# Kernel optimization log

Hardware: AMD Instinct MI355X
Metric: run time of the kernel (lower is better)

The kernel has to match this reference:

```python
import jax, jax.numpy as jnp
import numpy as np

B, S, P, E, H, NCTX = 4, 1024, 1024, 1024, 16, 2048
D = E // H


def setup_inputs() -> dict:
    key = jax.random.key(0)
    k0, k1, k2, k3 = jax.random.split(key, 4)
    x = jax.random.normal(k0, (B, S, E), jnp.float32)
    layer_past = jax.random.normal(k1, (2, B, H, P, D), jnp.float32)
    w_attn = jax.random.normal(k2, (E, 3 * E), jnp.float32) * 0.02
    b_attn = jnp.zeros((3 * E,), jnp.float32)
    w_proj = jax.random.normal(k3, (E, E), jnp.float32) * 0.02
    b_proj = jnp.zeros((E,), jnp.float32)
    return {"x": x, "layer_past": layer_past, "w_attn": w_attn,
            "b_attn": b_attn, "w_proj": w_proj, "b_proj": b_proj}


def reference(x, layer_past, w_attn, b_attn, w_proj, b_proj):
    # c_attn: Conv1D == linear with weight [nx, nf]
    qkv = x @ w_attn + b_attn                       # [B,S,3E]
    q, k, v = jnp.split(qkv, 3, axis=-1)

    def heads(t):                                   # [B,S,E] -> [B,H,S,D]
        return t.reshape(B, -1, H, D).transpose(0, 2, 1, 3)

    q, k, v = heads(q), heads(k), heads(v)
    # KV-cache concat: layer_past[0] is [B,H,P,D] (module transposes to
    # [B,H,D,P] then concats on last dim; equivalent to concat on seq dim).
    k = jnp.concatenate([layer_past[0], k], axis=2)  # [B,H,ns,D]
    v = jnp.concatenate([layer_past[1], v], axis=2)  # [B,H,ns,D]
    present = jnp.stack([k, v])                      # [2,B,H,ns,D]

    nd, ns = q.shape[2], k.shape[2]
    w = jnp.einsum('bhqd,bhkd->bhqk', q, k) / jnp.sqrt(jnp.float32(D))
    mask = jnp.tril(jnp.ones((NCTX, NCTX), jnp.float32))[ns - nd:ns, :ns]
    w = w * mask - 10000.0 * (1.0 - mask)
    a = jnp.einsum('bhqk,bhkd->bhqd', jax.nn.softmax(w, axis=-1), v)
    a = a.transpose(0, 2, 1, 3).reshape(B, -1, E)    # merge heads
    out = a @ w_proj + b_proj
    return out, present
```

## Files before the change

### kernel.cpp

```cpp
#include <hip/hip_runtime.h>
#include <hip/hip_bf16.h>

#define BB 4
#define SS 1024
#define PP 1024
#define EE 1024
#define HH 16
#define DD 64
#define NS 2048
#define E3 3072
#define VOFF 8388608
#define VPAST 4194304

typedef __attribute__((ext_vector_type(8))) short short8;
typedef __attribute__((ext_vector_type(4))) float floatx4;
typedef __attribute__((ext_vector_type(16))) float floatx16;
typedef __attribute__((ext_vector_type(4))) unsigned uintx4;

__device__ __forceinline__ short f2bf(float f) {
    return (short)(__bfloat16_as_ushort(__float2bfloat16(f)));
}

__device__ __forceinline__ unsigned cvtpk(float lo, float hi) {
    unsigned r;
    asm("v_cvt_pk_bf16_f32 %0, %1, %2" : "=v"(r) : "v"(lo), "v"(hi));
    return r;
}

__device__ __forceinline__ void plswap(unsigned &a, unsigned &b) {
    asm("v_permlane32_swap_b32 %0, %1" : "+v"(a), "+v"(b));
}

__device__ __forceinline__ void gload16(const void* g, void* l) {
    __builtin_amdgcn_global_load_lds(
        (const __attribute__((address_space(1))) void*)g,
        (__attribute__((address_space(3))) void*)l, 16, 0, 0);
}

__global__ __launch_bounds__(256) void cvt_copy_k(
    const float* __restrict__ x, const float* __restrict__ past,
    short* __restrict__ xb, short* __restrict__ kbp, short* __restrict__ vbp,
    float* __restrict__ present)
{
    size_t e0 = ((size_t)blockIdx.x * 256 + threadIdx.x) * 8;
    if (e0 < 4194304) {
        float4 a0 = *(const float4*)(x + e0);
        float4 a1 = *(const float4*)(x + e0 + 4);
        short8 s;
        s[0] = f2bf(a0.x); s[1] = f2bf(a0.y); s[2] = f2bf(a0.z); s[3] = f2bf(a0.w);
        s[4] = f2bf(a1.x); s[5] = f2bf(a1.y); s[6] = f2bf(a1.z); s[7] = f2bf(a1.w);
        *(short8*)(xb + e0) = s;
    } else {
        size_t r = e0 - 4194304;
        int sec = (r >= 4194304);
        if (sec) r -= 4194304;
        const float* src = past + (sec ? VPAST : 0) + r;
        int row = (int)(r >> 6);
        int bh = row >> 10, t = row & 1023, d = (int)(r & 63);
        size_t off = ((size_t)bh * NS + t) * DD + d;
        float4 a0 = *(const float4*)src;
        float4 a1 = *(const float4*)(src + 4);
        short8 s;
        s[0] = f2bf(a0.x); s[1] = f2bf(a0.y); s[2] = f2bf(a0.z); s[3] = f2bf(a0.w);
        s[4] = f2bf(a1.x); s[5] = f2bf(a1.y); s[6] = f2bf(a1.z); s[7] = f2bf(a1.w);
        *(short8*)((sec ? vbp : kbp) + off) = s;
        float* pd = present + (sec ? VOFF : 0) + off;
        *(float4*)(pd)     = a0;
        *(float4*)(pd + 4) = a1;
    }
}

__global__ __launch_bounds__(256) void wtrans_k(
    const float* __restrict__ wa, const float* __restrict__ wp,
    short* __restrict__ wab, short* __restrict__ wpb)
{
    __shared__ short Ts[64][72];
    int bid = blockIdx.x;
    const float* src; short* dst; int n0, k0, Nsrc;
    if (bid < 768) { k0 = (bid & 15) * 64; n0 = (bid >> 4) * 64; src = wa; dst = wab; Nsrc = E3; }
    else { bid -= 768; k0 = (bid & 15) * 64; n0 = (bid >> 4) * 64; src = wp; dst = wpb; Nsrc = EE; }
    int tid = threadIdx.x;
    int r = tid >> 2, c = (tid & 3) * 16;
    const float* s = src + (size_t)(k0 + r) * Nsrc + n0 + c;
    float4 a0 = *(const float4*)(s);
    float4 a1 = *(const float4*)(s + 4);
    float4 a2 = *(const float4*)(s + 8);
    float4 a3 = *(const float4*)(s + 12);
    Ts[c +  0][r] = f2bf(a0.x); Ts[c +  1][r] = f2bf(a0.y);
    Ts[c +  2][r] = f2bf(a0.z); Ts[c +  3][r] = f2bf(a0.w);
    Ts[c +  4][r] = f2bf(a1.x); Ts[c +  5][r] = f2bf(a1.y);
    Ts[c +  6][r] = f2bf(a1.z); Ts[c +  7][r] = f2bf(a1.w);
    Ts[c +  8][r] = f2bf(a2.x); Ts[c +  9][r] = f2bf(a2.y);
    Ts[c + 10][r] = f2bf(a2.z); Ts[c + 11][r] = f2bf(a2.w);
    Ts[c + 12][r] = f2bf(a3.x); Ts[c + 13][r] = f2bf(a3.y);
    Ts[c + 14][r] = f2bf(a3.z); Ts[c + 15][r] = f2bf(a3.w);
    __syncthreads();
    int n = tid >> 2, kc = (tid & 3) * 16;
    short8 v0 = *(const short8*)&Ts[n][kc];
    short8 v1 = *(const short8*)&Ts[n][kc + 8];
    short* d = dst + (size_t)(n0 + n) * EE + k0 + kc;
    *(short8*)d = v0;
    *(short8*)(d + 8) = v1;
}

template<int MODE>
__global__ __launch_bounds__(256) void gemm_bt_k(
    const short* __restrict__ A,
    const short* __restrict__ Bt,
    const float* __restrict__ bias,
    float* __restrict__ outf,
    short* __restrict__ qb, short* __restrict__ kbp, short* __restrict__ vbp,
    float* __restrict__ present,
    int N)
{
    __shared__ __align__(16) short As[128 * 32];
    __shared__ __align__(16) short Bs[128 * 32];
    int tid = threadIdx.x;
    int wave = tid >> 6, lane = tid & 63;
    int fr = lane & 15, quad = lane >> 4;
    int wm = wave >> 1, wn = wave & 1;
    int hw = blockIdx.y * gridDim.x + blockIdx.x;
    int nwg = gridDim.x * gridDim.y;
    int work = (hw & 7) * (nwg >> 3) + (hw >> 3);
    int bx = work / gridDim.y, by = work - bx * gridDim.y;
    int m0 = bx * 128, n0 = by * 128;

    floatx4 acc[4][4];
#pragma unroll
    for (int m = 0; m < 4; ++m)
#pragma unroll
        for (int n = 0; n < 4; ++n) acc[m][n] = (floatx4){0.f, 0.f, 0.f, 0.f};

    for (int k0 = 0; k0 < 1024; k0 += 32) {
        __syncthreads();
#pragma unroll
        for (int p = 0; p < 2; ++p) {
            int idx = p * 256 + tid;
            int row = idx >> 2, ch = idx & 3;
            gload16(A + (size_t)(m0 + row) * 1024 + k0 + ch * 8,
                    As + (p * 256 + wave * 64) * 8);
            gload16(Bt + (size_t)(n0 + row) * 1024 + k0 + ch * 8,
                    Bs + (p * 256 + wave * 64) * 8);
        }
        __syncthreads();
        short8 af[4], bf[4];
#pragma unroll
        for (int m = 0; m < 4; ++m)
            af[m] = *(const short8*)(As + (wm * 64 + m * 16 + fr) * 32 + quad * 8);
#pragma unroll
        for (int n = 0; n < 4; ++n)
            bf[n] = *(const short8*)(Bs + (wn * 64 + n * 16 + fr) * 32 + quad * 8);
#pragma unroll
        for (int m = 0; m < 4; ++m)
#pragma unroll
            for (int n = 0; n < 4; ++n)
                acc[m][n] = __builtin_amdgcn_mfma_f32_16x16x32_bf16(af[m], bf[n], acc[m][n], 0, 0, 0);
    }
#pragma unroll
    for (int n = 0; n < 4; ++n) {
        int gc = n0 + wn * 64 + n * 16 + fr;
        float bv = bias[gc];
#pragma unroll
        for (int m = 0; m < 4; ++m) {
#pragma unroll
            for (int r = 0; r < 4; ++r) {
                int gr = m0 + wm * 64 + m * 16 + quad * 4 + r;
                float val = acc[m][n][r] + bv;
                if (MODE == 1) {
                    outf[(size_t)gr * N + gc] = val;
                } else {
                    int sec = gc >> 10, h = (gc >> 6) & 15, d = gc & 63;
                    int b = gr >> 10, sq = gr & 1023;
                    size_t bh = (size_t)(b * HH + h);
                    if (sec == 0) {
                        qb[(bh * SS + sq) * DD + d] = f2bf(val * 0.125f);
                    } else {
                        size_t off = (bh * NS + PP + sq) * DD + d;
                        if (sec == 1) { present[off] = val;        kbp[off] = f2bf(val); }
                        else          { present[VOFF + off] = val; vbp[off] = f2bf(val); }
                    }
                }
            }
        }
    }
}

__global__ __launch_bounds__(256) void flash_attn_k(
    const short* __restrict__ qb, const short* __restrict__ kbp,
    const short* __restrict__ vbp, short* __restrict__ ab)
{
    __shared__ __align__(16) short smem[9216];
    short* Ks = smem;
    short* Vs = smem + 4096;

    int tid = threadIdx.x;
    int wave = tid >> 6, lane = tid & 63;
    int qcol = lane & 31, hi = lane >> 5;

    int bid = blockIdx.x;
    int work = (bid & 7) * 64 + (bid >> 3);
    int bh = work >> 3;
    int q0 = (work & 7) * 128;

    const short* qrow = qb + ((size_t)bh * SS + q0 + wave * 32 + qcol) * DD + hi * 8;
    short8 qf[4];
#pragma unroll
    for (int i = 0; i < 4; ++i) qf[i] = *(const short8*)(qrow + i * 16);

    const short* kbase = kbp + (size_t)bh * NS * DD;
    const short* vbase = vbp + (size_t)bh * NS * DD;

    float m_r = -1e30f, l_r = 0.f;
    floatx16 Oa[2];
#pragma unroll
    for (int dt = 0; dt < 2; ++dt)
#pragma unroll
        for (int r = 0; r < 16; ++r) Oa[dt][r] = 0.f;

    int vkey = lane, vd0 = wave * 16;
    int qminw = PP + q0 + wave * 32;
    int qmaxw = qminw + 31;
    const float L2E = 1.44269504f;

    int nchunks = 18 + (q0 >> 6);
    for (int c = 0; c < nchunks; ++c) {
        int t0 = c * 64;
        __syncthreads();
        const short* kc = kbase + (size_t)t0 * DD;
#pragma unroll
        for (int p = 0; p < 2; ++p) {
            int idx = p * 256 + tid;
            int row = idx >> 3, ch = idx & 7;
            gload16(kc + row * 64 + ((ch ^ (row & 7)) * 8),
                    Ks + (p * 256 + wave * 64) * 8);
        }
        {
            const short* src = vbase + ((size_t)t0 + vkey) * DD + vd0;
            short8 s0 = *(const short8*)src;
            short8 s1 = *(const short8*)(src + 8);
#pragma unroll
            for (int i = 0; i < 8; ++i) {
                Vs[(vd0 + i) * 72 + vkey] = s0[i];
                Vs[(vd0 + 8 + i) * 72 + vkey] = s1[i];
            }
        }
        __syncthreads();
        if (t0 > qmaxw) continue;

        floatx16 Sa[2];
#pragma unroll
        for (int ct = 0; ct < 2; ++ct)
#pragma unroll
            for (int r = 0; r < 16; ++r) Sa[ct][r] = 0.f;
#pragma unroll
        for (int ct = 0; ct < 2; ++ct) {
            int key = ct * 32 + qcol;
            int rbase = key * 64, rx = key & 7;
#pragma unroll
            for (int d0 = 0; d0 < 4; ++d0) {
                short8 kf = *(const short8*)(Ks + rbase + (((d0 * 2 + hi) ^ rx) * 8));
                Sa[ct] = __builtin_amdgcn_mfma_f32_32x32x16_bf16(kf, qf[d0], Sa[ct], 0, 0, 0);
            }
        }
        if (t0 + 63 > qminw) {
            int qa = qminw + qcol;
#pragma unroll
            for (int ct = 0; ct < 2; ++ct)
#pragma unroll
                for (int r = 0; r < 16; ++r) {
                    int ka = t0 + ct * 32 + (r & 3) + 8 * (r >> 2) + 4 * hi;
                    if (ka > qa) Sa[ct][r] = -1e30f;
                }
        }
        float mx0 = Sa[0][0], mx1 = Sa[0][1], mx2 = Sa[0][2], mx3 = Sa[0][3];
#pragma unroll
        for (int ct = 0; ct < 2; ++ct)
#pragma unroll
            for (int r = (ct ? 0 : 4); r < 16; r += 4) {
                mx0 = fmaxf(mx0, Sa[ct][r]);
                mx1 = fmaxf(mx1, Sa[ct][r + 1]);
                mx2 = fmaxf(mx2, Sa[ct][r + 2]);
                mx3 = fmaxf(mx3, Sa[ct][r + 3]);
            }
        float mx = fmaxf(fmaxf(mx0, mx1), fmaxf(mx2, mx3));
        mx = fmaxf(mx, __shfl_xor(mx, 32, 64));
        float mnew = fmaxf(m_r, mx);
        float base = mnew * L2E;
        float s0 = 0.f, s1 = 0.f, s2 = 0.f, s3 = 0.f;
#pragma unroll
        for (int ct = 0; ct < 2; ++ct)
#pragma unroll
            for (int r = 0; r < 16; r += 4) {
                float p0 = exp2f(Sa[ct][r] * L2E - base);
                float p1 = exp2f(Sa[ct][r + 1] * L2E - base);
                float p2 = exp2f(Sa[ct][r + 2] * L2E - base);
                float p3 = exp2f(Sa[ct][r + 3] * L2E - base);
                Sa[ct][r] = p0; Sa[ct][r + 1] = p1; Sa[ct][r + 2] = p2; Sa[ct][r + 3] = p3;
                s0 += p0; s1 += p1; s2 += p2; s3 += p3;
            }
        float sum = (s0 + s1) + (s2 + s3);
        sum += __shfl_xor(sum, 32, 64);
        float alpha = exp2f(m_r * L2E - base);
        l_r = l_r * alpha + sum;
        m_r = mnew;
#pragma unroll
        for (int dt = 0; dt < 2; ++dt)
#pragma unroll
            for (int r = 0; r < 16; ++r) Oa[dt][r] *= alpha;

        short8 pfr[2][2];
#pragma unroll
        for (int ct = 0; ct < 2; ++ct) {
            unsigned w0 = cvtpk(Sa[ct][0],  Sa[ct][1]);
            unsigned w2 = cvtpk(Sa[ct][4],  Sa[ct][5]);
            unsigned w1 = cvtpk(Sa[ct][2],  Sa[ct][3]);
            unsigned w3 = cvtpk(Sa[ct][6],  Sa[ct][7]);
            plswap(w0, w2);
            plswap(w1, w3);
            union { uintx4 u; short8 s; } cv0;
            cv0.u = (uintx4){w0, w1, w2, w3};
            pfr[ct][0] = cv0.s;
            unsigned x0 = cvtpk(Sa[ct][8],  Sa[ct][9]);
            unsigned x2 = cvtpk(Sa[ct][12], Sa[ct][13]);
            unsigned x1 = cvtpk(Sa[ct][10], Sa[ct][11]);
            unsigned x3 = cvtpk(Sa[ct][14], Sa[ct][15]);
            plswap(x0, x2);
            plswap(x1, x3);
            union { uintx4 u; short8 s; } cv1;
            cv1.u = (uintx4){x0, x1, x2, x3};
            pfr[ct][1] = cv1.s;
        }
#pragma unroll
        for (int ct = 0; ct < 2; ++ct)
#pragma unroll
            for (int ks = 0; ks < 2; ++ks) {
                int keyb = ct * 32 + ks * 16 + hi * 8;
#pragma unroll
                for (int dt = 0; dt < 2; ++dt) {
                    short8 vf = *(const short8*)(Vs + (dt * 32 + qcol) * 72 + keyb);
                    Oa[dt] = __builtin_amdgcn_mfma_f32_32x32x16_bf16(vf, pfr[ct][ks], Oa[dt], 0, 0, 0);
                }
            }
    }
    __syncthreads();
    short* Ow = smem + wave * 2304;
    float inv = 1.f / l_r;
#pragma unroll
    for (int dt = 0; dt < 2; ++dt)
#pragma unroll
        for (int r = 0; r < 16; ++r) {
            int d = dt * 32 + (r & 3) + 8 * (r >> 2) + 4 * hi;
            Ow[qcol * 72 + d] = f2bf(Oa[dt][r] * inv);
        }
    int b = bh >> 4, h = bh & 15;
    int row = lane >> 1, doff = (lane & 1) * 32;
    int qa = q0 + wave * 32 + row;
    short* dst = ab + ((size_t)(b * SS + qa)) * EE + h * DD + doff;
    const short* srcr = Ow + row * 72 + doff;
    *(short8*)(dst)      = *(const short8*)(srcr);
    *(short8*)(dst + 8)  = *(const short8*)(srcr + 8);
    *(short8*)(dst + 16) = *(const short8*)(srcr + 16);
    *(short8*)(dst + 24) = *(const short8*)(srcr + 24);
}

extern "C" void kernel_launch(void* const* d_in, const int* in_sizes, int n_in,
                              void* d_out, int out_size, void* d_ws, size_t ws_size,
                              hipStream_t stream) {
    const float* x      = (const float*)d_in[0];
    const float* past   = (const float*)d_in[1];
    const float* w_attn = (const float*)d_in[2];
    const float* b_attn = (const float*)d_in[3];
    const float* w_proj = (const float*)d_in[4];
    const float* b_proj = (const float*)d_in[5];
    float* out = (float*)d_out;
    float* present = out + (size_t)BB * SS * EE;

    short* ws  = (short*)d_ws;
    short* xb  = ws;
    short* wab = xb  + 4194304;
    short* wpb = wab + 3145728;
    short* qb  = wpb + 1048576;
    short* kbp = qb  + 4194304;
    short* vbp = kbp + 8388608;
    short* ab  = vbp + 8388608;

    cvt_copy_k<<<6144, 256, 0, stream>>>(x, past, xb, kbp, vbp, present);
    wtrans_k<<<1024, 256, 0, stream>>>(w_attn, w_proj, wab, wpb);
    gemm_bt_k<0><<<dim3(32, 24), 256, 0, stream>>>(xb, wab, b_attn, nullptr,
                                                   qb, kbp, vbp, present, E3);
    flash_attn_k<<<512, 256, 0, stream>>>(qb, kbp, vbp, ab);
    gemm_bt_k<1><<<dim3(32, 8), 256, 0, stream>>>(ab, wpb, b_proj, out,
                                                  nullptr, nullptr, nullptr, nullptr, EE);
}
```

Before: 311.6 us.

## Double-buffer flash-attention K/V, swizzle V tile, lazy rescale, narrower proj GEMM tiles

The flash-attention loop now double-buffers K and V in shared memory. It prefetches the next chunk's K via async loads and V into registers while computing on the current chunk, which removes one barrier per iteration. V gets an XOR-swizzled layout in place of the padded one. The log2(e) factor is folded into the Q scale, and the softmax running max is only rescaled when a wave's new max exceeds the old one by a threshold, which skips most alpha multiplies. The output projection GEMM uses 128x64 tiles and twice as many blocks to fill more CUs, and the larger LDS footprint may lower attention occupancy.

```diff
diff --git a/kernel.cpp b/kernel.cpp
--- a/kernel.cpp
+++ b/kernel.cpp
@@ -103,7 +103,7 @@
     *(short8*)(d + 8) = v1;
 }
 
-template<int MODE>
+template<int MODE, int NT>
 __global__ __launch_bounds__(256) void gemm_bt_k(
     const short* __restrict__ A,
     const short* __restrict__ Bt,
@@ -113,21 +113,23 @@
     float* __restrict__ present,
     int N)
 {
+    constexpr int MR = (NT == 128) ? 4 : 2;
     __shared__ __align__(16) short As[128 * 32];
-    __shared__ __align__(16) short Bs[128 * 32];
+    __shared__ __align__(16) short Bs[NT * 32];
     int tid = threadIdx.x;
     int wave = tid >> 6, lane = tid & 63;
     int fr = lane & 15, quad = lane >> 4;
-    int wm = wave >> 1, wn = wave & 1;
+    int wm = (NT == 128) ? (wave >> 1) : wave;
+    int wn = (NT == 128) ? (wave & 1) : 0;
     int hw = blockIdx.y * gridDim.x + blockIdx.x;
     int nwg = gridDim.x * gridDim.y;
     int work = (hw & 7) * (nwg >> 3) + (hw >> 3);
     int bx = work / gridDim.y, by = work - bx * gridDim.y;
-    int m0 = bx * 128, n0 = by * 128;
-
-    floatx4 acc[4][4];
-#pragma unroll
-    for (int m = 0; m < 4; ++m)
+    int m0 = bx * 128, n0 = by * NT;
+
+    floatx4 acc[MR][4];
+#pragma unroll
+    for (int m = 0; m < MR; ++m)
 #pragma unroll
         for (int n = 0; n < 4; ++n) acc[m][n] = (floatx4){0.f, 0.f, 0.f, 0.f};
 
@@ -139,19 +141,24 @@
             int row = idx >> 2, ch = idx & 3;
             gload16(A + (size_t)(m0 + row) * 1024 + k0 + ch * 8,
                     As + (p * 256 + wave * 64) * 8);
+        }
+#pragma unroll
+        for (int p = 0; p < NT / 64; ++p) {
+            int idx = p * 256 + tid;
+            int row = idx >> 2, ch = idx & 3;
             gload16(Bt + (size_t)(n0 + row) * 1024 + k0 + ch * 8,
                     Bs + (p * 256 + wave * 64) * 8);
         }
         __syncthreads();
-        short8 af[4], bf[4];
-#pragma unroll
-        for (int m = 0; m < 4; ++m)
-            af[m] = *(const short8*)(As + (wm * 64 + m * 16 + fr) * 32 + quad * 8);
+        short8 af[MR], bf[4];
+#pragma unroll
+        for (int m = 0; m < MR; ++m)
+            af[m] = *(const short8*)(As + (wm * (MR * 16) + m * 16 + fr) * 32 + quad * 8);
 #pragma unroll
         for (int n = 0; n < 4; ++n)
             bf[n] = *(const short8*)(Bs + (wn * 64 + n * 16 + fr) * 32 + quad * 8);
 #pragma unroll
-        for (int m = 0; m < 4; ++m)
+        for (int m = 0; m < MR; ++m)
 #pragma unroll
             for (int n = 0; n < 4; ++n)
                 acc[m][n] = __builtin_amdgcn_mfma_f32_16x16x32_bf16(af[m], bf[n], acc[m][n], 0, 0, 0);
@@ -161,10 +168,10 @@
         int gc = n0 + wn * 64 + n * 16 + fr;
         float bv = bias[gc];
 #pragma unroll
-        for (int m = 0; m < 4; ++m) {
+        for (int m = 0; m < MR; ++m) {
 #pragma unroll
             for (int r = 0; r < 4; ++r) {
-                int gr = m0 + wm * 64 + m * 16 + quad * 4 + r;
+                int gr = m0 + wm * (MR * 16) + m * 16 + quad * 4 + r;
                 float val = acc[m][n][r] + bv;
                 if (MODE == 1) {
                     outf[(size_t)gr * N + gc] = val;
@@ -173,7 +180,7 @@
                     int b = gr >> 10, sq = gr & 1023;
                     size_t bh = (size_t)(b * HH + h);
                     if (sec == 0) {
-                        qb[(bh * SS + sq) * DD + d] = f2bf(val * 0.125f);
+                        qb[(bh * SS + sq) * DD + d] = f2bf(val * 0.18033688f);
                     } else {
                         size_t off = (bh * NS + PP + sq) * DD + d;
                         if (sec == 1) { present[off] = val;        kbp[off] = f2bf(val); }
@@ -189,9 +196,9 @@
     const short* __restrict__ qb, const short* __restrict__ kbp,
     const short* __restrict__ vbp, short* __restrict__ ab)
 {
-    __shared__ __align__(16) short smem[9216];
+    __shared__ __align__(16) short smem[16384];
     short* Ks = smem;
-    short* Vs = smem + 4096;
+    short* Vs = smem + 8192;
 
     int tid = threadIdx.x;
     int wave = tid >> 6, lane = tid & 63;
@@ -217,132 +224,149 @@
 #pragma unroll
         for (int r = 0; r < 16; ++r) Oa[dt][r] = 0.f;
 
-    int vkey = lane, vd0 = wave * 16;
+    int vkey = lane, vd0 = (tid >> 6) * 16;
     int qminw = PP + q0 + wave * 32;
     int qmaxw = qminw + 31;
-    const float L2E = 1.44269504f;
 
     int nchunks = 18 + (q0 >> 6);
-    for (int c = 0; c < nchunks; ++c) {
-        int t0 = c * 64;
-        __syncthreads();
-        const short* kc = kbase + (size_t)t0 * DD;
+    short8 vs0, vs1;
+
+    auto KISSUE = [&](int cc, int bufi) {
+        const short* kc = kbase + (size_t)cc * 64 * DD;
+        short* Kd = Ks + bufi * 4096;
 #pragma unroll
         for (int p = 0; p < 2; ++p) {
             int idx = p * 256 + tid;
             int row = idx >> 3, ch = idx & 7;
-            gload16(kc + row * 64 + ((ch ^ (row & 7)) * 8),
-                    Ks + (p * 256 + wave * 64) * 8);
-        }
-        {
-            const short* src = vbase + ((size_t)t0 + vkey) * DD + vd0;
-            short8 s0 = *(const short8*)src;
-            short8 s1 = *(const short8*)(src + 8);
-#pragma unroll
-            for (int i = 0; i < 8; ++i) {
-                Vs[(vd0 + i) * 72 + vkey] = s0[i];
-                Vs[(vd0 + 8 + i) * 72 + vkey] = s1[i];
-            }
-        }
-        __syncthreads();
-        if (t0 > qmaxw) continue;
-
-        floatx16 Sa[2];
-#pragma unroll
-        for (int ct = 0; ct < 2; ++ct)
-#pragma unroll
-            for (int r = 0; r < 16; ++r) Sa[ct][r] = 0.f;
-#pragma unroll
-        for (int ct = 0; ct < 2; ++ct) {
-            int key = ct * 32 + qcol;
-            int rbase = key * 64, rx = key & 7;
-#pragma unroll
-            for (int d0 = 0; d0 < 4; ++d0) {
-                short8 kf = *(const short8*)(Ks + rbase + (((d0 * 2 + hi) ^ rx) * 8));
-                Sa[ct] = __builtin_amdgcn_mfma_f32_32x32x16_bf16(kf, qf[d0], Sa[ct], 0, 0, 0);
-            }
-        }
-        if (t0 + 63 > qminw) {
-            int qa = qminw + qcol;
+            gload16(kc + row * 64 + ((ch ^ (row & 7)) * 8), Kd + (p * 256 + wave * 64) * 8);
+        }
+    };
+    auto VLOAD = [&](int cc) {
+        const short* src = vbase + ((size_t)cc * 64 + vkey) * DD + vd0;
+        vs0 = *(const short8*)src;
+        vs1 = *(const short8*)(src + 8);
+    };
+    auto VWRITE = [&](int bufi) {
+        short* Vd = Vs + bufi * 4096;
+#pragma unroll
+        for (int i = 0; i < 8; ++i) {
+            int d0i = vd0 + i, d1i = vd0 + 8 + i;
+            Vd[d0i * 64 + (((vkey >> 3) ^ (d0i & 7)) << 3) + (vkey & 7)] = vs0[i];
+            Vd[d1i * 64 + (((vkey >> 3) ^ (d1i & 7)) << 3) + (vkey & 7)] = vs1[i];
+        }
+    };
+
+    KISSUE(0, 0); VLOAD(0); VWRITE(0);
+    __syncthreads();
+
+    for (int c = 0; c < nchunks; ++c) {
+        int t0 = c * 64;
+        int cur = c & 1;
+        KISSUE(c + 1, cur ^ 1);
+        VLOAD(c + 1);
+        if (t0 <= qmaxw) {
+            const short* Kc = Ks + cur * 4096;
+            const short* Vc = Vs + cur * 4096;
+            floatx16 Sa[2];
 #pragma unroll
             for (int ct = 0; ct < 2; ++ct)
 #pragma unroll
-                for (int r = 0; r < 16; ++r) {
-                    int ka = t0 + ct * 32 + (r & 3) + 8 * (r >> 2) + 4 * hi;
-                    if (ka > qa) Sa[ct][r] = -1e30f;
-                }
-        }
-        float mx0 = Sa[0][0], mx1 = Sa[0][1], mx2 = Sa[0][2], mx3 = Sa[0][3];
-#pragma unroll
-        for (int ct = 0; ct < 2; ++ct)
-#pragma unroll
-            for (int r = (ct ? 0 : 4); r < 16; r += 4) {
-                mx0 = fmaxf(mx0, Sa[ct][r]);
-                mx1 = fmaxf(mx1, Sa[ct][r + 1]);
-                mx2 = fmaxf(mx2, Sa[ct][r + 2]);
-                mx3 = fmaxf(mx3, Sa[ct][r + 3]);
-            }
-        float mx = fmaxf(fmaxf(mx0, mx1), fmaxf(mx2, mx3));
-        mx = fmaxf(mx, __shfl_xor(mx, 32, 64));
-        float mnew = fmaxf(m_r, mx);
-        float base = mnew * L2E;
-        float s0 = 0.f, s1 = 0.f, s2 = 0.f, s3 = 0.f;
-#pragma unroll
-        for (int ct = 0; ct < 2; ++ct)
-#pragma unroll
-            for (int r = 0; r < 16; r += 4) {
-                float p0 = exp2f(Sa[ct][r] * L2E - base);
-                float p1 = exp2f(Sa[ct][r + 1] * L2E - base);
-                float p2 = exp2f(Sa[ct][r + 2] * L2E - base);
-                float p3 = exp2f(Sa[ct][r + 3] * L2E - base);
-                Sa[ct][r] = p0; Sa[ct][r + 1] = p1; Sa[ct][r + 2] = p2; Sa[ct][r + 3] = p3;
-                s0 += p0; s1 += p1; s2 += p2; s3 += p3;
-            }
-        float sum = (s0 + s1) + (s2 + s3);
-        sum += __shfl_xor(sum, 32, 64);
-        float alpha = exp2f(m_r * L2E - base);
-        l_r = l_r * alpha + sum;
-        m_r = mnew;
-#pragma unroll
-        for (int dt = 0; dt < 2; ++dt)
-#pragma unroll
-            for (int r = 0; r < 16; ++r) Oa[dt][r] *= alpha;
-
-        short8 pfr[2][2];
-#pragma unroll
-        for (int ct = 0; ct < 2; ++ct) {
-            unsigned w0 = cvtpk(Sa[ct][0],  Sa[ct][1]);
-            unsigned w2 = cvtpk(Sa[ct][4],  Sa[ct][5]);
-            unsigned w1 = cvtpk(Sa[ct][2],  Sa[ct][3]);
-            unsigned w3 = cvtpk(Sa[ct][6],  Sa[ct][7]);
-            plswap(w0, w2);
-            plswap(w1, w3);
-            union { uintx4 u; short8 s; } cv0;
-            cv0.u = (uintx4){w0, w1, w2, w3};
-            pfr[ct][0] = cv0.s;
-            unsigned x0 = cvtpk(Sa[ct][8],  Sa[ct][9]);
-            unsigned x2 = cvtpk(Sa[ct][12], Sa[ct][13]);
-            unsigned x1 = cvtpk(Sa[ct][10], Sa[ct][11]);
-            unsigned x3 = cvtpk(Sa[ct][14], Sa[ct][15]);
-            plswap(x0, x2);
-            plswap(x1, x3);
-            union { uintx4 u; short8 s; } cv1;
-            cv1.u = (uintx4){x0, x1, x2, x3};
-            pfr[ct][1] = cv1.s;
-        }
-#pragma unroll
-        for (int ct = 0; ct < 2; ++ct)
-#pragma unroll
-            for (int ks = 0; ks < 2; ++ks) {
-                int keyb = ct * 32 + ks * 16 + hi * 8;
-#pragma unroll
-                for (int dt = 0; dt < 2; ++dt) {
-                    short8 vf = *(const short8*)(Vs + (dt * 32 + qcol) * 72 + keyb);
-                    Oa[dt] = __builtin_amdgcn_mfma_f32_32x32x16_bf16(vf, pfr[ct][ks], Oa[dt], 0, 0, 0);
+                for (int r = 0; r < 16; ++r) Sa[ct][r] = 0.f;
+#pragma unroll
+            for (int ct = 0; ct < 2; ++ct) {
+                int key = ct * 32 + qcol;
+                int rbase = key * 64, rx = key & 7;
+#pragma unroll
+                for (int d0 = 0; d0 < 4; ++d0) {
+                    short8 kf = *(const short8*)(Kc + rbase + (((d0 * 2 + hi) ^ rx) * 8));
+                    Sa[ct] = __builtin_amdgcn_mfma_f32_32x32x16_bf16(kf, qf[d0], Sa[ct], 0, 0, 0);
                 }
             }
+            if (t0 + 63 > qminw) {
+                int qa = qminw + qcol;
+#pragma unroll
+                for (int ct = 0; ct < 2; ++ct)
+#pragma unroll
+                    for (int r = 0; r < 16; ++r) {
+                        int ka = t0 + ct * 32 + (r & 3) + 8 * (r >> 2) + 4 * hi;
+                        if (ka > qa) Sa[ct][r] = -1e30f;
+                    }
+            }
+            float mx0 = Sa[0][0], mx1 = Sa[0][1], mx2 = Sa[0][2], mx3 = Sa[0][3];
+#pragma unroll
+            for (int ct = 0; ct < 2; ++ct)
+#pragma unroll
+                for (int r = (ct ? 0 : 4); r < 16; r += 4) {
+                    mx0 = fmaxf(mx0, Sa[ct][r]);
+                    mx1 = fmaxf(mx1, Sa[ct][r + 1]);
+                    mx2 = fmaxf(mx2, Sa[ct][r + 2]);
+                    mx3 = fmaxf(mx3, Sa[ct][r + 3]);
+                }
+            float mx = fmaxf(fmaxf(mx0, mx1), fmaxf(mx2, mx3));
+            mx = fmaxf(mx, __shfl_xor(mx, 32, 64));
+            if (!__all(mx <= m_r + 11.5416f)) {
+                float mnew = fmaxf(m_r, mx);
+                float al = exp2f(m_r - mnew);
+                l_r *= al;
+#pragma unroll
+                for (int dt = 0; dt < 2; ++dt)
+#pragma unroll
+                    for (int r = 0; r < 16; ++r) Oa[dt][r] *= al;
+                m_r = mnew;
+            }
+            float s0 = 0.f, s1 = 0.f, s2 = 0.f, s3 = 0.f;
+#pragma unroll
+            for (int ct = 0; ct < 2; ++ct)
+#pragma unroll
+                for (int r = 0; r < 16; r += 4) {
+                    float p0 = exp2f(Sa[ct][r]     - m_r);
+                    float p1 = exp2f(Sa[ct][r + 1] - m_r);
+                    float p2 = exp2f(Sa[ct][r + 2] - m_r);
+                    float p3 = exp2f(Sa[ct][r + 3] - m_r);
+                    Sa[ct][r] = p0; Sa[ct][r + 1] = p1; Sa[ct][r + 2] = p2; Sa[ct][r + 3] = p3;
+                    s0 += p0; s1 += p1; s2 += p2; s3 += p3;
+                }
+            float sum = (s0 + s1) + (s2 + s3);
+            sum += __shfl_xor(sum, 32, 64);
+            l_r += sum;
+            short8 pfr[2][2];
+#pragma unroll
+            for (int ct = 0; ct < 2; ++ct) {
+                unsigned w0 = cvtpk(Sa[ct][0],  Sa[ct][1]);
+                unsigned w2 = cvtpk(Sa[ct][4],  Sa[ct][5]);
+                unsigned w1 = cvtpk(Sa[ct][2],  Sa[ct][3]);
+                unsigned w3 = cvtpk(Sa[ct][6],  Sa[ct][7]);
+                plswap(w0, w2);
+                plswap(w1, w3);
+                union { uintx4 u; short8 s; } cv0;
+                cv0.u = (uintx4){w0, w1, w2, w3};
+                pfr[ct][0] = cv0.s;
+                unsigned x0 = cvtpk(Sa[ct][8],  Sa[ct][9]);
+                unsigned x2 = cvtpk(Sa[ct][12], Sa[ct][13]);
+                unsigned x1 = cvtpk(Sa[ct][10], Sa[ct][11]);
+                unsigned x3 = cvtpk(Sa[ct][14], Sa[ct][15]);
+                plswap(x0, x2);
+                plswap(x1, x3);
+                union { uintx4 u; short8 s; } cv1;
+                cv1.u = (uintx4){x0, x1, x2, x3};
+                pfr[ct][1] = cv1.s;
+            }
+#pragma unroll
+            for (int ct = 0; ct < 2; ++ct)
+#pragma unroll
+                for (int ks = 0; ks < 2; ++ks) {
+                    int chunkb = ct * 4 + ks * 2 + hi;
+#pragma unroll
+                    for (int dt = 0; dt < 2; ++dt) {
+                        int row = dt * 32 + qcol;
+                        short8 vf = *(const short8*)(Vc + row * 64 + ((chunkb ^ (row & 7)) << 3));
+                        Oa[dt] = __builtin_amdgcn_mfma_f32_32x32x16_bf16(vf, pfr[ct][ks], Oa[dt], 0, 0, 0);
+                    }
+                }
+        }
+        VWRITE(cur ^ 1);
+        __syncthreads();
     }
-    __syncthreads();
     short* Ow = smem + wave * 2304;
     float inv = 1.f / l_r;
 #pragma unroll
@@ -386,9 +410,9 @@
 
     cvt_copy_k<<<6144, 256, 0, stream>>>(x, past, xb, kbp, vbp, present);
     wtrans_k<<<1024, 256, 0, stream>>>(w_attn, w_proj, wab, wpb);
-    gemm_bt_k<0><<<dim3(32, 24), 256, 0, stream>>>(xb, wab, b_attn, nullptr,
-                                                   qb, kbp, vbp, present, E3);
+    gemm_bt_k<0, 128><<<dim3(32, 24), 256, 0, stream>>>(xb, wab, b_attn, nullptr,
+                                                        qb, kbp, vbp, present, E3);
     flash_attn_k<<<512, 256, 0, stream>>>(qb, kbp, vbp, ab);
-    gemm_bt_k<1><<<dim3(32, 8), 256, 0, stream>>>(ab, wpb, b_proj, out,
-                                                  nullptr, nullptr, nullptr, nullptr, EE);
-}
+    gemm_bt_k<1, 64><<<dim3(32, 16), 256, 0, stream>>>(ab, wpb, b_proj, out,
+                                                       nullptr, nullptr, nullptr, nullptr, EE);
+}
```

New measurement: 302.4 us. 3.0% less time.
